# Performance work log

Hardware: AMD Instinct MI355X
Metric: run time of the kernel (lower is better)

The kernel has to match this reference:

```python
import jax, jax.numpy as jnp
import numpy as np

N_NODES = 50000


def gin_conv(x, src, dst, W, b, eps=0.0):
    # GINConv: nn((1+eps)*x_i + sum_{j in N(i)} x_j)
    agg = jax.ops.segment_sum(x[src], dst, num_segments=N_NODES)  # [N, D]
    h = (1.0 + eps) * x + agg
    return h @ W + b


def setup_inputs() -> dict:
    key = jax.random.key(0)
    ks = jax.random.split(key, 8)
    n, e = N_NODES, 800000
    d_in, d_h, d_out = 128, 128, 64
    feature = jax.random.normal(ks[0], (n, d_in), dtype=jnp.float32)
    edge_index = jax.random.randint(ks[1], (2, e), 0, n, dtype=jnp.int64)
    s1 = 1.0 / np.sqrt(d_in)
    sh = 1.0 / np.sqrt(d_h)
    W1 = jax.random.normal(ks[2], (d_in, d_h), dtype=jnp.float32) * s1
    b1 = jnp.zeros((d_h,), dtype=jnp.float32)
    Wh = jax.random.normal(ks[3], (d_h, d_h), dtype=jnp.float32) * sh
    bh = jnp.zeros((d_h,), dtype=jnp.float32)
    Wo = jax.random.normal(ks[4], (d_h, d_out), dtype=jnp.float32) * sh
    bo = jnp.zeros((d_out,), dtype=jnp.float32)
    return {"feature": feature, "edge_index": edge_index, "W1": W1, "b1": b1,
            "Wh": Wh, "bh": bh, "Wo": Wo, "bo": bo}


def reference(feature, edge_index, W1, b1, Wh, bh, Wo, bo):
    src, dst = edge_index[0], edge_index[1]
    x = gin_conv(feature, src, dst, W1, b1)
    x = jax.nn.relu(x)
    # one hidden layer (layer_num=3); dropout disabled (eval)
    x = gin_conv(x, src, dst, Wh, bh)
    x = jax.nn.relu(x)
    x = gin_conv(x, src, dst, Wo, bo)
    return jax.nn.log_softmax(x, axis=1)
```

## Files before the change

### kernel.cpp

```cpp
#include <hip/hip_runtime.h>

typedef short short8 __attribute__((ext_vector_type(8)));
typedef float f32x4 __attribute__((ext_vector_type(4)));


__device__ inline unsigned short f2bf(float f) {
    union { float f; unsigned u; } v; v.f = f;
    unsigned r = v.u + 0x7fffu + ((v.u >> 16) & 1u);
    return (unsigned short)(r >> 16);
}
__device__ inline unsigned pack2(float a, float b) {
    return (unsigned)f2bf(a) | ((unsigned)f2bf(b) << 16);
}
__device__ inline float bflo(unsigned u) { union { unsigned q; float f; } c; c.q = u << 16; return c.f; }
__device__ inline float bfhi(unsigned u) { union { unsigned q; float f; } c; c.q = u & 0xffff0000u; return c.f; }

#define ACC8(vv)                                     \
    acc[0] += bflo(vv.x); acc[1] += bfhi(vv.x);      \
    acc[2] += bflo(vv.y); acc[3] += bfhi(vv.y);      \
    acc[4] += bflo(vv.z); acc[5] += bfhi(vv.z);      \
    acc[6] += bflo(vv.w); acc[7] += bfhi(vv.w);

template <int TPN, typename F>
__device__ __forceinline__ void gather_acc(float acc[8], const uint4* __restrict__ x,
                                           int lane, int beg, int end, F geti) {
    int k = beg;
    for (; k + 16 <= end; k += 16) {
        int idx[16];
#pragma unroll
        for (int j = 0; j < 16; j++) idx[j] = geti(k + j);
        uint4 v[16];
#pragma unroll
        for (int j = 0; j < 16; j++) v[j] = x[(size_t)idx[j] * TPN + lane];
#pragma unroll
        for (int j = 0; j < 16; j++) { ACC8(v[j]) }
    }
    int r = end - k;
    if (r > 0) {
        int lim = end - 1;
        int idx[16];
#pragma unroll
        for (int j = 0; j < 16; j++) idx[j] = geti(min(k + j, lim));
        uint4 v[16];
#pragma unroll
        for (int j = 0; j < 16; j++) v[j] = x[(size_t)idx[j] * TPN + lane];
#pragma unroll
        for (int j = 0; j < 16; j++) {
            if (k + j < end) { ACC8(v[j]) }
        }
    }
}


#define EPB 2048
#define NE 8
#define BSH 9
#define MAXBKT 128
#define DCAP 10240

__global__ __launch_bounds__(256) void mega1(const int* __restrict__ dst, int* __restrict__ cnt2d,
                                             int e, int nbkt, int nblk,
                                             const float4* __restrict__ feat, uint2* __restrict__ featb,
                                             int cvtb, int nf4,
                                             const float* __restrict__ W1, const float* __restrict__ Wh,
                                             const float* __restrict__ Wo,
                                             unsigned short* __restrict__ W1t, unsigned short* __restrict__ Wht,
                                             unsigned short* __restrict__ Wot) {
    __shared__ int hist[MAXBKT];
    int t = threadIdx.x, b = blockIdx.x;
    if (b < nblk) {
        for (int j = t; j < nbkt; j += 256) hist[j] = 0;
        __syncthreads();
        int base = b * EPB;
#pragma unroll
        for (int j = 0; j < NE; j++) {
            int idx = base + t + 256 * j;
            if (idx < e) atomicAdd(&hist[dst[idx] >> BSH], 1);
        }
        __syncthreads();
        for (int j = t; j < nbkt; j += 256) cnt2d[j * nblk + b] = hist[j];
    } else if (b < nblk + cvtb) {
        int i = (b - nblk) * 256 + t;
        if (i < nf4) {
            float4 v = feat[i];
            featb[i] = make_uint2(pack2(v.x, v.y), pack2(v.z, v.w));
        }
    } else {
        int i = (b - nblk - cvtb) * 256 + t;
        if (i < 16384) {
            int k = i >> 7, nn = i & 127;
            W1t[nn * 128 + k] = f2bf(W1[i]);
        } else if (i < 32768) {
            int j = i - 16384, k = j >> 7, nn = j & 127;
            Wht[nn * 128 + k] = f2bf(Wh[j]);
        } else if (i < 40960) {
            int j = i - 32768, k = j >> 6, nn = j & 63;
            Wot[nn * 128 + k] = f2bf(Wo[j]);
        }
    }
}

__global__ __launch_bounds__(512) void scanB1(int* __restrict__ cnt2d, int* __restrict__ totals, int nblk) {
    __shared__ int s[512];
    int t = threadIdx.x, b = blockIdx.x;
    int v = (t < nblk) ? cnt2d[b * nblk + t] : 0;
    s[t] = v;
    __syncthreads();
    for (int off = 1; off < 512; off <<= 1) {
        int u = (t >= off) ? s[t - off] : 0;
        __syncthreads();
        s[t] += u;
        __syncthreads();
    }
    if (t < nblk) cnt2d[b * nblk + t] = s[t] - v;
    if (t == nblk - 1) totals[b] = s[t];
}

__global__ __launch_bounds__(128) void scanB2(const int* __restrict__ totals, int* __restrict__ bbase,
                                              int* __restrict__ row_ptr, int nbkt, int n, int e) {
    __shared__ int s[128];
    int t = threadIdx.x;
    int v = (t < nbkt) ? totals[t] : 0;
    s[t] = v;
    __syncthreads();
    for (int off = 1; off < 128; off <<= 1) {
        int u = (t >= off) ? s[t - off] : 0;
        __syncthreads();
        s[t] += u;
        __syncthreads();
    }
    if (t < nbkt) bbase[t] = s[t] - v;
    if (t == 0) row_ptr[n] = e;
}

__global__ __launch_bounds__(256) void binC(const int* __restrict__ src, const int* __restrict__ dst,
                                            const int* __restrict__ cnt2d, const int* __restrict__ bbase,
                                            unsigned* __restrict__ pairs, int e, int nbkt, int nblk) {
    __shared__ int hist[MAXBKT], loff[MAXBKT], cur[MAXBKT], gb[MAXBKT];
    __shared__ int sc[256];
    __shared__ unsigned sorted[EPB];
    int t = threadIdx.x, blk = blockIdx.x;
    for (int b = t; b < nbkt; b += 256) hist[b] = 0;
    __syncthreads();
    int base = blk * EPB;
    int cnt = min(EPB, e - base);
    unsigned packed[NE];
    int bb[NE];
#pragma unroll
    for (int j = 0; j < NE; j++) {
        int idx = base + t + 256 * j;
        bb[j] = -1;
        if (idx < e) {
            unsigned s0 = (unsigned)src[idx], d = (unsigned)dst[idx];
            int b = (int)(d >> BSH);
            bb[j] = b;
            packed[j] = s0 | ((d & ((1u << BSH) - 1)) << 16) | ((unsigned)b << 25);
            atomicAdd(&hist[b], 1);
        }
    }
    __syncthreads();
    int v = (t < nbkt) ? hist[t] : 0;
    sc[t] = v;
    __syncthreads();
    for (int off = 1; off < 256; off <<= 1) {
        int u = (t >= off) ? sc[t - off] : 0;
        __syncthreads();
        sc[t] += u;
        __syncthreads();
    }
    if (t < nbkt) {
        int ex = sc[t] - v;
        loff[t] = ex;
        cur[t] = ex;
        gb[t] = bbase[t] + cnt2d[t * nblk + blk];
    }
    __syncthreads();
#pragma unroll
    for (int j = 0; j < NE; j++) {
        if (bb[j] >= 0) {
            int r = atomicAdd(&cur[bb[j]], 1);
            sorted[r] = packed[j];
        }
    }
    __syncthreads();
    for (int i = t; i < cnt; i += 256) {
        unsigned w = sorted[i];
        int b = (int)(w >> 25);
        pairs[gb[b] + (i - loff[b])] = w;
    }
}

__global__ __launch_bounds__(512) void buildD(const unsigned* __restrict__ pairs,
                                              const int* __restrict__ totals, const int* __restrict__ bbase,
                                              int* __restrict__ row_ptr, unsigned short* __restrict__ csr, int n) {
    __shared__ int hist[512], off[512];
    __shared__ unsigned short lcsr[DCAP];
    int t = threadIdx.x, b = blockIdx.x;
    int cnt = totals[b], base = bbase[b];
    hist[t] = 0;
    __syncthreads();
    for (int i = t; i < cnt; i += 512)
        atomicAdd(&hist[(pairs[base + i] >> 16) & 511], 1);
    __syncthreads();
    int v = hist[t];
    off[t] = v;
    __syncthreads();
    for (int o = 1; o < 512; o <<= 1) {
        int u = (t >= o) ? off[t - o] : 0;
        __syncthreads();
        off[t] += u;
        __syncthreads();
    }
    int excl = off[t] - v;
    int node = (b << BSH) + t;
    if (node < n) row_ptr[node] = base + excl;
    __syncthreads();
    hist[t] = excl;
    __syncthreads();
    for (int i = t; i < cnt; i += 512) {
        unsigned w = pairs[base + i];
        int r = atomicAdd(&hist[(w >> 16) & 511], 1);
        if (r < DCAP) lcsr[r] = (unsigned short)(w & 0xFFFFu);
    }
    __syncthreads();
    int lim = min(cnt, DCAP);
    for (int i = t; i < lim; i += 512) csr[base + i] = lcsr[i];
}


#define ECAP 1024

template <bool SECOND>
__global__ __launch_bounds__(256) void fused_layer(
    const uint4* __restrict__ x, const int* __restrict__ row_ptr,
    const unsigned short* __restrict__ csr,
    const short8* __restrict__ Bt, const float* __restrict__ bias,
    unsigned short* __restrict__ out_h,
    const short8* __restrict__ Bt2,
    unsigned short* __restrict__ out_y,
    int n) {
    __shared__ unsigned short As[16][136];
    __shared__ unsigned short Hs[SECOND ? 16 : 1][SECOND ? 136 : 1];
    __shared__ unsigned short eidx[ECAP];

    int t = threadIdx.x;
    int nl = t >> 4, chunk = t & 15;
    int r0 = blockIdx.x * 16;
    int node = r0 + nl;

    int beg = 0, end = 0;
    uint4 s0 = make_uint4(0u, 0u, 0u, 0u);
    if (node < n) {
        beg = row_ptr[node];
        end = row_ptr[node + 1];
        s0 = x[(size_t)node * 16 + chunk];
    }

    int E0 = row_ptr[r0];
    int E1 = row_ptr[min(r0 + 16, n)];
    int ecnt = min(E1 - E0, ECAP);
    for (int i = t; i < ecnt; i += 256) eidx[i] = csr[E0 + i];
    __syncthreads();

    float acc[8] = {0.f, 0.f, 0.f, 0.f, 0.f, 0.f, 0.f, 0.f};
    if (node < n) {
        ACC8(s0)
        if (end - E0 <= ECAP) {
            gather_acc<16>(acc, x, chunk, beg - E0, end - E0,
                           [&](int k) { return (int)eidx[k]; });
        } else {
            gather_acc<16>(acc, x, chunk, beg, end,
                           [&](int k) { return (int)csr[k]; });
        }
    }
    uint4 packed;
    packed.x = pack2(acc[0], acc[1]); packed.y = pack2(acc[2], acc[3]);
    packed.z = pack2(acc[4], acc[5]); packed.w = pack2(acc[6], acc[7]);
    ((uint4*)&As[nl][0])[chunk] = packed;
    __syncthreads();

    int wid = t >> 6, lane = t & 63;
    int lm = lane & 15, lq = lane >> 4;

    short8 a[4];
#pragma unroll
    for (int kc = 0; kc < 4; kc++)
        a[kc] = *(const short8*)&As[lm][kc * 32 + lq * 8];

    f32x4 hacc[2];
#pragma unroll
    for (int nt = 0; nt < 2; nt++) hacc[nt] = (f32x4){0.f, 0.f, 0.f, 0.f};
#pragma unroll
    for (int nt = 0; nt < 2; nt++) {
        const short8* Br = Bt + (size_t)((wid * 2 + nt) * 16 + lm) * 16;
#pragma unroll
        for (int kc = 0; kc < 4; kc++)
            hacc[nt] = __builtin_amdgcn_mfma_f32_16x16x32_bf16(a[kc], Br[kc * 4 + lq], hacc[nt], 0, 0, 0);
    }

#pragma unroll
    for (int nt = 0; nt < 2; nt++) {
        int col = (wid * 2 + nt) * 16 + lm;
        float bv = bias[col];
#pragma unroll
        for (int i = 0; i < 4; i++) {
            int row = r0 + lq * 4 + i;
            float v = fmaxf(hacc[nt][i] + bv, 0.f);
            if (SECOND) {
                Hs[lq * 4 + i][col] = f2bf(v);
            } else if (row < n) {
                out_h[(size_t)row * 128 + col] = f2bf(v);
            }
        }
    }

    if (SECOND) {
        __syncthreads();
        short8 a2[4];
#pragma unroll
        for (int kc = 0; kc < 4; kc++)
            a2[kc] = *(const short8*)&Hs[lm][kc * 32 + lq * 8];
        f32x4 yacc = (f32x4){0.f, 0.f, 0.f, 0.f};
        const short8* Br2 = Bt2 + (size_t)(wid * 16 + lm) * 16;
#pragma unroll
        for (int kc = 0; kc < 4; kc++)
            yacc = __builtin_amdgcn_mfma_f32_16x16x32_bf16(a2[kc], Br2[kc * 4 + lq], yacc, 0, 0, 0);
        int col = wid * 16 + lm;
#pragma unroll
        for (int i = 0; i < 4; i++) {
            int row = r0 + lq * 4 + i;
            if (row < n) out_y[(size_t)row * 64 + col] = f2bf(yacc[i]);
        }
    }
}


#define ECAP2 1536

__global__ __launch_bounds__(256) void agg_lsm(
    const uint4* __restrict__ x, float* __restrict__ out,
    const int* __restrict__ row_ptr, const unsigned short* __restrict__ csr,
    const float* __restrict__ bo, int n) {
    __shared__ unsigned short eidx[ECAP2];
    int t = threadIdx.x;
    int r0 = blockIdx.x * 32;
    int node = r0 + (t >> 3), lane = t & 7;

    int beg = 0, end = 0;
    uint4 s0 = make_uint4(0u, 0u, 0u, 0u);
    if (node < n) {
        beg = row_ptr[node];
        end = row_ptr[node + 1];
        s0 = x[(size_t)node * 8 + lane];
    }

    int E0 = row_ptr[r0];
    int E1 = row_ptr[min(r0 + 32, n)];
    int ecnt = min(E1 - E0, ECAP2);
    for (int i = t; i < ecnt; i += 256) eidx[i] = csr[E0 + i];
    __syncthreads();

    if (node >= n) return;
    float acc[8] = { bflo(s0.x), bfhi(s0.x), bflo(s0.y), bfhi(s0.y),
                     bflo(s0.z), bfhi(s0.z), bflo(s0.w), bfhi(s0.w) };
    if (end - E0 <= ECAP2) {
        gather_acc<8>(acc, x, lane, beg - E0, end - E0,
                      [&](int k) { return (int)eidx[k]; });
    } else {
        gather_acc<8>(acc, x, lane, beg, end,
                      [&](int k) { return (int)csr[k]; });
    }

    const float4* bo4 = (const float4*)bo;
    float4 bA = bo4[lane * 2], bB = bo4[lane * 2 + 1];
    acc[0] += bA.x; acc[1] += bA.y; acc[2] += bA.z; acc[3] += bA.w;
    acc[4] += bB.x; acc[5] += bB.y; acc[6] += bB.z; acc[7] += bB.w;
    float m = acc[0];
#pragma unroll
    for (int j = 1; j < 8; j++) m = fmaxf(m, acc[j]);
#pragma unroll
    for (int off = 1; off < 8; off <<= 1) m = fmaxf(m, __shfl_xor(m, off, 64));
    float s = 0.f;
#pragma unroll
    for (int j = 0; j < 8; j++) s += __expf(acc[j] - m);
#pragma unroll
    for (int off = 1; off < 8; off <<= 1) s += __shfl_xor(s, off, 64);
    float ls = m + __logf(s);
    float4 o0 = make_float4(acc[0] - ls, acc[1] - ls, acc[2] - ls, acc[3] - ls);
    float4 o1 = make_float4(acc[4] - ls, acc[5] - ls, acc[6] - ls, acc[7] - ls);
    float4* op = (float4*)(out + (size_t)node * 64 + lane * 8);
    op[0] = o0;
    op[1] = o1;
}


extern "C" void kernel_launch(void* const* d_in, const int* in_sizes, int n_in,
                              void* d_out, int out_size, void* d_ws, size_t ws_size,
                              hipStream_t stream) {
    const float* feature = (const float*)d_in[0];
    const int*   edges   = (const int*)d_in[1];
    const float* W1 = (const float*)d_in[2];
    const float* b1 = (const float*)d_in[3];
    const float* Wh = (const float*)d_in[4];
    const float* bh = (const float*)d_in[5];
    const float* Wo = (const float*)d_in[6];
    const float* bo = (const float*)d_in[7];

    int n = in_sizes[0] / 128;
    int e = in_sizes[1] / 2;
    const int* src = edges;
    const int* dst = edges + e;

    int nbkt = (n + 511) >> BSH;
    int nblk = (e + EPB - 1) / EPB;
    int nf4 = n * 32;
    int cvtb = (nf4 + 255) / 256;

    char* ws = (char*)d_ws;
    auto take = [&](size_t bytes) {
        char* p = ws;
        ws += (bytes + 255) & ~(size_t)255;
        return p;
    };
    int* cnt2d   = (int*)take((size_t)nbkt * nblk * 4);
    int* totals  = (int*)take((size_t)nbkt * 4);
    int* bbase   = (int*)take((size_t)(nbkt + 1) * 4);
    int* row_ptr = (int*)take((size_t)(n + 1) * 4);
    unsigned* pairs = (unsigned*)take((size_t)e * 4);
    unsigned short* csr = (unsigned short*)take((size_t)e * 2);
    unsigned short* featb = (unsigned short*)take((size_t)n * 128 * 2);
    unsigned short* hb    = (unsigned short*)take((size_t)n * 128 * 2);
    unsigned short* yb    = (unsigned short*)take((size_t)n * 64 * 2);
    unsigned short* W1t = (unsigned short*)take(128 * 128 * 2);
    unsigned short* Wht = (unsigned short*)take(128 * 128 * 2);
    unsigned short* Wot = (unsigned short*)take(64 * 128 * 2);

    mega1<<<nblk + cvtb + 160, 256, 0, stream>>>(
        dst, cnt2d, e, nbkt, nblk,
        (const float4*)feature, (uint2*)featb, cvtb, nf4,
        W1, Wh, Wo, W1t, Wht, Wot);
    scanB1<<<nbkt, 512, 0, stream>>>(cnt2d, totals, nblk);
    scanB2<<<1, 128, 0, stream>>>(totals, bbase, row_ptr, nbkt, n, e);
    binC<<<nblk, 256, 0, stream>>>(src, dst, cnt2d, bbase, pairs, e, nbkt, nblk);
    buildD<<<nbkt, 512, 0, stream>>>(pairs, totals, bbase, row_ptr, csr, n);

    int fblocks = (n + 15) / 16;

    fused_layer<false><<<fblocks, 256, 0, stream>>>(
        (const uint4*)featb, row_ptr, csr, (const short8*)W1t, b1,
        hb, nullptr, nullptr, n);

    fused_layer<true><<<fblocks, 256, 0, stream>>>(
        (const uint4*)hb, row_ptr, csr, (const short8*)Wht, bh,
        nullptr, (const short8*)Wot, yb, n);

    agg_lsm<<<(n + 31) / 32, 256, 0, stream>>>(
        (const uint4*)yb, (float*)d_out, row_ptr, csr, bo, n);
}
```

Measured before the change: 208.2 us.

## Split aggregation from GEMM and shard feature columns across XCDs

```diff
diff --git a/kernel.cpp b/kernel.cpp
--- a/kernel.cpp
+++ b/kernel.cpp
@@ -228,12 +228,80 @@
 }
 
 
-#define ECAP 1024
-
-template <bool SECOND>
-__global__ __launch_bounds__(256) void fused_layer(
+#define ECAP3 2048
+
+template <int TPN, int NSH, int NSPLIT, bool OUTF32>
+__global__ __launch_bounds__(256) void agg_shard(
     const uint4* __restrict__ x, const int* __restrict__ row_ptr,
     const unsigned short* __restrict__ csr,
+    uint4* __restrict__ outb,
+    float4* __restrict__ outf,
+    int n, int ngrp) {
+    static_assert(NSH * NSPLIT == 8, "groups must equal XCD count");
+    __shared__ unsigned short eidx[ECAP3];
+
+    int t = threadIdx.x;
+    int g = blockIdx.x & 7;
+    int s = g % NSH, sp = g / NSH;
+    int q = blockIdx.x >> 3;
+    int ns = (n + NSPLIT - 1) / NSPLIT;
+    int sbeg = sp * ns, send = min(sbeg + ns, n);
+    int r0 = sbeg + q * 64;
+    if (r0 >= send) return;
+    int r1 = min(r0 + 64, send);
+
+    {
+        int W = (n * 4 + ngrp - 1) / ngrp;
+        int w0 = q * W, w1 = min(w0 + W, n * 4);
+        unsigned wacc = 0;
+        for (int j = w0 + t; j < w1; j += 256) {
+            uint4 wv = x[(size_t)(j >> 2) * TPN + s * 4 + (j & 3)];
+            wacc ^= wv.x ^ wv.y ^ wv.z ^ wv.w;
+        }
+        asm volatile("" :: "v"(wacc));
+    }
+
+    int E0 = row_ptr[r0];
+    int E1 = row_ptr[r1];
+    int ecnt = E1 - E0;
+    bool fits = (ecnt <= ECAP3);
+    int scnt = fits ? ecnt : ECAP3;
+    for (int i = t; i < scnt; i += 256) eidx[i] = csr[E0 + i];
+    __syncthreads();
+
+    int node = r0 + (t >> 2), c = t & 3;
+    int lane = s * 4 + c;
+    if (node >= r1) return;
+
+    float acc[8] = {0.f, 0.f, 0.f, 0.f, 0.f, 0.f, 0.f, 0.f};
+    uint4 sv = x[(size_t)node * TPN + lane];
+    ACC8(sv)
+    int beg = row_ptr[node], end = row_ptr[node + 1];
+    if (fits) {
+        gather_acc<TPN>(acc, x, lane, beg - E0, end - E0,
+                        [&](int k) { return (int)eidx[k]; });
+    } else {
+        gather_acc<TPN>(acc, x, lane, beg, end,
+                        [&](int k) { return (int)csr[k]; });
+    }
+
+    if (OUTF32) {
+        float4 o0 = make_float4(acc[0], acc[1], acc[2], acc[3]);
+        float4 o1 = make_float4(acc[4], acc[5], acc[6], acc[7]);
+        outf[((size_t)node * TPN + lane) * 2]     = o0;
+        outf[((size_t)node * TPN + lane) * 2 + 1] = o1;
+    } else {
+        uint4 p;
+        p.x = pack2(acc[0], acc[1]); p.y = pack2(acc[2], acc[3]);
+        p.z = pack2(acc[4], acc[5]); p.w = pack2(acc[6], acc[7]);
+        outb[(size_t)node * TPN + lane] = p;
+    }
+}
+
+
+template <bool SECOND>
+__global__ __launch_bounds__(256) void gemm_dense(
+    const uint4* __restrict__ A,
     const short8* __restrict__ Bt, const float* __restrict__ bias,
     unsigned short* __restrict__ out_h,
     const short8* __restrict__ Bt2,
@@ -241,42 +309,13 @@
     int n) {
     __shared__ unsigned short As[16][136];
     __shared__ unsigned short Hs[SECOND ? 16 : 1][SECOND ? 136 : 1];
-    __shared__ unsigned short eidx[ECAP];
 
     int t = threadIdx.x;
-    int nl = t >> 4, chunk = t & 15;
     int r0 = blockIdx.x * 16;
-    int node = r0 + nl;
-
-    int beg = 0, end = 0;
-    uint4 s0 = make_uint4(0u, 0u, 0u, 0u);
-    if (node < n) {
-        beg = row_ptr[node];
-        end = row_ptr[node + 1];
-        s0 = x[(size_t)node * 16 + chunk];
-    }
-
-    int E0 = row_ptr[r0];
-    int E1 = row_ptr[min(r0 + 16, n)];
-    int ecnt = min(E1 - E0, ECAP);
-    for (int i = t; i < ecnt; i += 256) eidx[i] = csr[E0 + i];
-    __syncthreads();
-
-    float acc[8] = {0.f, 0.f, 0.f, 0.f, 0.f, 0.f, 0.f, 0.f};
-    if (node < n) {
-        ACC8(s0)
-        if (end - E0 <= ECAP) {
-            gather_acc<16>(acc, x, chunk, beg - E0, end - E0,
-                           [&](int k) { return (int)eidx[k]; });
-        } else {
-            gather_acc<16>(acc, x, chunk, beg, end,
-                           [&](int k) { return (int)csr[k]; });
-        }
-    }
-    uint4 packed;
-    packed.x = pack2(acc[0], acc[1]); packed.y = pack2(acc[2], acc[3]);
-    packed.z = pack2(acc[4], acc[5]); packed.w = pack2(acc[6], acc[7]);
-    ((uint4*)&As[nl][0])[chunk] = packed;
+    int lr = t >> 4, c = t & 15;
+    uint4 av = make_uint4(0u, 0u, 0u, 0u);
+    if (r0 + lr < n) av = A[(size_t)(r0 + lr) * 16 + c];
+    ((uint4*)&As[lr][0])[c] = av;
     __syncthreads();
 
     int wid = t >> 6, lane = t & 63;
@@ -335,41 +374,16 @@
 }
 
 
-#define ECAP2 1536
-
-__global__ __launch_bounds__(256) void agg_lsm(
-    const uint4* __restrict__ x, float* __restrict__ out,
-    const int* __restrict__ row_ptr, const unsigned short* __restrict__ csr,
+__global__ __launch_bounds__(256) void lsm_k(
+    const float4* __restrict__ A3, float* __restrict__ out,
     const float* __restrict__ bo, int n) {
-    __shared__ unsigned short eidx[ECAP2];
     int t = threadIdx.x;
-    int r0 = blockIdx.x * 32;
-    int node = r0 + (t >> 3), lane = t & 7;
-
-    int beg = 0, end = 0;
-    uint4 s0 = make_uint4(0u, 0u, 0u, 0u);
-    if (node < n) {
-        beg = row_ptr[node];
-        end = row_ptr[node + 1];
-        s0 = x[(size_t)node * 8 + lane];
-    }
-
-    int E0 = row_ptr[r0];
-    int E1 = row_ptr[min(r0 + 32, n)];
-    int ecnt = min(E1 - E0, ECAP2);
-    for (int i = t; i < ecnt; i += 256) eidx[i] = csr[E0 + i];
-    __syncthreads();
-
+    int node = blockIdx.x * 32 + (t >> 3), lane = t & 7;
     if (node >= n) return;
-    float acc[8] = { bflo(s0.x), bfhi(s0.x), bflo(s0.y), bfhi(s0.y),
-                     bflo(s0.z), bfhi(s0.z), bflo(s0.w), bfhi(s0.w) };
-    if (end - E0 <= ECAP2) {
-        gather_acc<8>(acc, x, lane, beg - E0, end - E0,
-                      [&](int k) { return (int)eidx[k]; });
-    } else {
-        gather_acc<8>(acc, x, lane, beg, end,
-                      [&](int k) { return (int)csr[k]; });
-    }
+
+    float4 v0 = A3[(size_t)node * 16 + lane * 2];
+    float4 v1 = A3[(size_t)node * 16 + lane * 2 + 1];
+    float acc[8] = {v0.x, v0.y, v0.z, v0.w, v1.x, v1.y, v1.z, v1.w};
 
     const float4* bo4 = (const float4*)bo;
     float4 bA = bo4[lane * 2], bB = bo4[lane * 2 + 1];
@@ -431,9 +445,11 @@
     unsigned short* featb = (unsigned short*)take((size_t)n * 128 * 2);
     unsigned short* hb    = (unsigned short*)take((size_t)n * 128 * 2);
     unsigned short* yb    = (unsigned short*)take((size_t)n * 64 * 2);
+    unsigned short* A1    = (unsigned short*)take((size_t)n * 128 * 2);
     unsigned short* W1t = (unsigned short*)take(128 * 128 * 2);
     unsigned short* Wht = (unsigned short*)take(128 * 128 * 2);
     unsigned short* Wot = (unsigned short*)take(64 * 128 * 2);
+    float* A3f = (float*)featb;
 
     mega1<<<nblk + cvtb + 160, 256, 0, stream>>>(
         dst, cnt2d, e, nbkt, nblk,
@@ -444,16 +460,22 @@
     binC<<<nblk, 256, 0, stream>>>(src, dst, cnt2d, bbase, pairs, e, nbkt, nblk);
     buildD<<<nbkt, 512, 0, stream>>>(pairs, totals, bbase, row_ptr, csr, n);
 
-    int fblocks = (n + 15) / 16;
-
-    fused_layer<false><<<fblocks, 256, 0, stream>>>(
-        (const uint4*)featb, row_ptr, csr, (const short8*)W1t, b1,
-        hb, nullptr, nullptr, n);
-
-    fused_layer<true><<<fblocks, 256, 0, stream>>>(
-        (const uint4*)hb, row_ptr, csr, (const short8*)Wht, bh,
-        nullptr, (const short8*)Wot, yb, n);
-
-    agg_lsm<<<(n + 31) / 32, 256, 0, stream>>>(
-        (const uint4*)yb, (float*)d_out, row_ptr, csr, bo, n);
-}
+    int gblocks = (n + 15) / 16;
+    int ngrp1 = (((n + 1) / 2) + 63) / 64;
+    int ngrp3 = (((n + 3) / 4) + 63) / 64;
+
+    agg_shard<16, 4, 2, false><<<8 * ngrp1, 256, 0, stream>>>(
+        (const uint4*)featb, row_ptr, csr, (uint4*)A1, nullptr, n, ngrp1);
+    gemm_dense<false><<<gblocks, 256, 0, stream>>>(
+        (const uint4*)A1, (const short8*)W1t, b1, hb, nullptr, nullptr, n);
+
+    agg_shard<16, 4, 2, false><<<8 * ngrp1, 256, 0, stream>>>(
+        (const uint4*)hb, row_ptr, csr, (uint4*)A1, nullptr, n, ngrp1);
+    gemm_dense<true><<<gblocks, 256, 0, stream>>>(
+        (const uint4*)A1, (const short8*)Wht, bh, nullptr, (const short8*)Wot, yb, n);
+
+    agg_shard<8, 2, 4, true><<<8 * ngrp3, 256, 0, stream>>>(
+        (const uint4*)yb, row_ptr, csr, nullptr, (float4*)A3f, n, ngrp3);
+    lsm_k<<<(n + 31) / 32, 256, 0, stream>>>(
+        (const float4*)A3f, (float*)d_out, bo, n);
+}
```

Result: slower. 261.8 us (+25.7%).
